# Kernel tuning notes

Measured on AMD Instinct MI355X. Metric: run time of the kernel, lower is better.

Reference implementation:

```python
import jax, jax.numpy as jnp
import numpy as np

DIM, H, WH, WW = 192, 6, 8, 8
N = WH * WW
B = 4096
NW = 64
HALF = DIM // 2
HD = DIM // H


def _make_buffers():
    # continuous relative coords table (1, 2WH-1, 2WW-1, 2), Swin-V2 style
    rh = np.arange(-(WH - 1), WH, dtype=np.float32)
    rw = np.arange(-(WW - 1), WW, dtype=np.float32)
    gh, gw = np.meshgrid(rh, rw, indexing='ij')
    tab = np.stack([gh, gw], axis=-1)[None]  # (1, 2WH-1, 2WW-1, 2)
    tab[..., 0] /= WH - 1
    tab[..., 1] /= WW - 1
    tab *= 3.2
    tab = np.sign(tab) * (1.0 - np.exp(-np.abs(tab)))
    # relative position index (N, N) int
    ch, cw = np.meshgrid(np.arange(WH), np.arange(WW), indexing='ij')
    coords = np.stack([ch, cw]).reshape(2, -1)  # (2, N)
    rel = coords[:, :, None] - coords[:, None, :]  # (2, N, N)
    rel = rel.transpose(1, 2, 0).astype(np.int64)
    rel[:, :, 0] += WH - 1
    rel[:, :, 1] += WW - 1
    rel[:, :, 0] *= 2 * WW - 1
    idx = rel.sum(-1)  # (N, N)
    return jnp.asarray(tab, jnp.float32), jnp.asarray(idx, jnp.int32)


def setup_inputs() -> dict:
    key = jax.random.key(0)
    ks = jax.random.split(key, 24)
    w = lambda k, shape: jax.random.normal(k, shape, jnp.float32) * 0.02
    rpb_table, rp_index = _make_buffers()
    inp = {
        'x': jax.random.normal(ks[0], (B, N, DIM), jnp.float32),
        'mask': jnp.zeros((NW, N, N), jnp.float32),
        'logit_scale': jnp.log(10.0) * jnp.ones((H, 1, 1), jnp.float32),
        'mlp_w1': w(ks[1], (128, 2)), 'mlp_b1': jnp.zeros((128,), jnp.float32),
        'mlp_w2': w(ks[2], (H, 128)),
        'q1w': w(ks[3], (HALF, HALF)), 'q1b': jnp.zeros((HALF,), jnp.float32),
        'q2w': w(ks[4], (HALF, HALF)), 'q2b': jnp.zeros((HALF,), jnp.float32),
        'k1w': w(ks[5], (HALF, HALF)), 'k1b': jnp.zeros((HALF,), jnp.float32),
        'k2w': w(ks[6], (HALF, HALF)), 'k2b': jnp.zeros((HALF,), jnp.float32),
        'v1w': w(ks[7], (HALF, HALF)), 'v1b': jnp.zeros((HALF,), jnp.float32),
        'v2w': w(ks[8], (HALF, HALF)), 'v2b': jnp.zeros((HALF,), jnp.float32),
        'p1w': w(ks[9], (HALF, HALF)), 'p1b': jnp.zeros((HALF,), jnp.float32),
        'p2w': w(ks[10], (HALF, HALF)), 'p2b': jnp.zeros((HALF,), jnp.float32),
        'rpb_table': rpb_table,
        'rp_index': rp_index,
    }
    return inp


def _lin(x, w, b):
    return x @ w.T + b


def _l2n(x):
    return x / jnp.maximum(jnp.linalg.norm(x, axis=-1, keepdims=True), 1e-12)


def reference(x, mask, logit_scale, mlp_w1, mlp_b1, mlp_w2,
              q1w, q1b, q2w, q2b, k1w, k1b, k2w, k2b, v1w, v1b, v2w, v2b,
              p1w, p1b, p2w, p2b, rpb_table, rp_index):
    b, n, c = x.shape
    h, hd = H, c // H
    x0, x1 = x[..., :c // 2], x[..., c // 2:]
    # split-channel GRL residual projections, then concat halves -> heads
    def heads(y0w, y0b, y1w, y1b):
        y = jnp.concatenate([x0 + _lin(x0, y0w, y0b), x1 + _lin(x1, y1w, y1b)], -1)
        return y.reshape(b, n, h, hd).transpose(0, 2, 1, 3)  # (b, h, n, hd)
    q = heads(q1w, q1b, q2w, q2b)
    k = heads(k1w, k1b, k2w, k2b)
    v = heads(v1w, v1b, v2w, v2b)
    # cosine attention with learned per-head logit scale
    attn = jnp.einsum('bhnd,bhmd->bhnm', _l2n(q), _l2n(k))
    scale = jnp.exp(jnp.minimum(logit_scale, jnp.log(jnp.float32(100.0))))  # (h,1,1)
    attn = attn * scale
    # ESRPB: MLP over continuous relative coords -> per-head bias
    tab = jax.nn.relu(rpb_table @ mlp_w1.T + mlp_b1) @ mlp_w2.T  # (1, 2WH-1, 2WW-1, h)
    tab = tab.reshape(-1, h)
    rpb = tab[rp_index.reshape(-1)].reshape(n, n, h).transpose(2, 0, 1)  # (h, n, n)
    attn = attn + 16.0 * jax.nn.sigmoid(rpb)[None]
    nw = mask.shape[0]
    attn = (attn.reshape(b // nw, nw, h, n, n) + mask[None, :, None]).reshape(b, h, n, n)
    attn = jax.nn.softmax(attn, axis=-1)
    out = jnp.einsum('bhnm,bhmd->bhnd', attn, v).transpose(0, 2, 1, 3).reshape(b, n, c)
    o0, o1 = out[..., :c // 2], out[..., c // 2:]
    return jnp.concatenate([_lin(o0, p1w, p1b), _lin(o1, p2w, p2b)], -1)
```

## Files before the change

kernel.cpp:

```cpp
#include <hip/hip_runtime.h>
#include <hip/hip_bf16.h>

#define NT 64
#define DM 192

typedef __attribute__((ext_vector_type(4))) float f32x4;
typedef __attribute__((ext_vector_type(4))) float float4v;
using half2v = __attribute__((ext_vector_type(2))) _Float16;
using half4v = __attribute__((ext_vector_type(4))) _Float16;

#define BIAS_OFF  147456
#define TAB_OFF   6438912
#define SCALE_OFF 6444312

__device__ __forceinline__ half4v pk4(float a, float b, float c, float d){
  half2v lo = __builtin_bit_cast(half2v, __builtin_amdgcn_cvt_pkrtz(a, b));
  half2v hi = __builtin_bit_cast(half2v, __builtin_amdgcn_cvt_pkrtz(c, d));
  half4v r; r[0]=lo[0]; r[1]=lo[1]; r[2]=hi[0]; r[3]=hi[1];
  return r;
}

__global__ __launch_bounds__(384) void pre_a(
  const float* __restrict__ q1w, const float* __restrict__ q2w,
  const float* __restrict__ k1w, const float* __restrict__ k2w,
  const float* __restrict__ v1w, const float* __restrict__ v2w,
  const float* __restrict__ p1w, const float* __restrict__ p2w,
  const float* __restrict__ w1, const float* __restrict__ b1,
  const float* __restrict__ w2, const float* __restrict__ rpbt,
  const float* __restrict__ ls, char* __restrict__ ws)
{
  int blk = blockIdx.x, t = threadIdx.x;
  if (blk < 48) {
    const float* Ws[8] = {q1w,q2w,k1w,k2w,v1w,v2w,p1w,p2w};
    int mat = blk / 6, ct = blk % 6;
    int lane = t & 63, ks = t >> 6;
    const float* W = Ws[mat];
    int c  = 16*ct + (lane & 15);
    int d0 = 16*ks + 4*(lane >> 4);
    half4v h;
    #pragma unroll
    for (int j = 0; j < 4; ++j) h[j] = (_Float16)W[c*96 + d0 + j];
    *(half4v*)(ws + (size_t)((mat*6+ct)*6+ks)*512 + lane*8) = h;
  } else {
    float* tab = (float*)(ws + TAB_OFF);
    if (t < 225) {
      float t0 = rpbt[2*t], t1 = rpbt[2*t+1];
      float acc[6] = {0,0,0,0,0,0};
      for (int j = 0; j < 128; ++j) {
        float hv = fmaxf(t0*w1[2*j] + t1*w1[2*j+1] + b1[j], 0.f);
        #pragma unroll
        for (int hh = 0; hh < 6; ++hh) acc[hh] += hv * w2[hh*128 + j];
      }
      #pragma unroll
      for (int hh = 0; hh < 6; ++hh) tab[t*6 + hh] = acc[hh];
    }
    if (t >= 240 && t < 246) {
      float* sc = (float*)(ws + SCALE_OFF);
      int i = t - 240;
      sc[i] = expf(fminf(ls[i], 4.605170185988091f));
    }
  }
}

__global__ __launch_bounds__(256) void pre_b(
  const float* __restrict__ mask, const int* __restrict__ rpi,
  char* __restrict__ ws)
{
  int w = blockIdx.x / 6, h = blockIdx.x % 6;
  int lane = threadIdx.x & 63, nt = threadIdx.x >> 6;
  const float* tab = (const float*)(ws + TAB_OFF);
  float* bias = (float*)(ws + BIAS_OFF);
  #pragma unroll
  for (int mt = 0; mt < 4; ++mt)
    #pragma unroll
    for (int r = 0; r < 4; ++r) {
      int m = 16*mt + ((lane >> 4) << 2) + r;
      int n = 16*nt + (lane & 15);
      int idx = rpi[n*64 + m];
      float tv = tab[idx*6 + h];
      float sg = 16.f / (1.f + expf(-tv));
      float mv = mask[(w*64 + n)*64 + m];
      bias[(size_t)(((w*6+h)*4+mt)*4+nt)*256 + lane*4 + r] = sg + mv;
    }
}

__global__ __launch_bounds__(768, 2) void win_attn(
  const float* __restrict__ x, const char* __restrict__ ws,
  const float* __restrict__ q1b, const float* __restrict__ q2b,
  const float* __restrict__ k1b, const float* __restrict__ k2b,
  const float* __restrict__ v1b, const float* __restrict__ v2b,
  const float* __restrict__ p1b, const float* __restrict__ p2b,
  float* __restrict__ out)
{
  __shared__ __align__(16) _Float16 xo2[2][64*200];
  const int tid = threadIdx.x;
  const int wv = tid >> 6, lane = tid & 63;
  const int llo = lane & 15, lhi = lane >> 4;
  const int wgrp = (wv >= 6) ? 1 : 0;
  const int h = wv - 6*wgrp;
  const int b = blockIdx.x*2 + wgrp, w_in = b & 63;
  const int lt = tid - 384*wgrp;
  _Float16* xo = xo2[wgrp];
  const int half = (h < 3) ? 0 : 1;
  const int hd0 = 32 * (h % 3);
  const f32x4 zf = {0.f,0.f,0.f,0.f};
  const float* xg = x + (size_t)b * (NT*DM);

  float4v xv[8];
  #pragma unroll
  for (int it = 0; it < 8; ++it) xv[it] = *(const float4v*)(xg + 4*(lt + it*384));
  #pragma unroll
  for (int it = 0; it < 8; ++it) {
    int f4 = lt + it*384;
    int row = f4 / 48, c4 = f4 % 48;
    *(half4v*)(xo + row*200 + c4*4) = pk4(xv[it][0], xv[it][1], xv[it][2], xv[it][3]);
  }
  __syncthreads();

  f32x4 qacc[2][4], kacc[2][4];
  #pragma unroll
  for (int dt = 0; dt < 2; ++dt)
    #pragma unroll
    for (int tt = 0; tt < 4; ++tt) { qacc[dt][tt] = zf; kacc[dt][tt] = zf; }
  #pragma unroll
  for (int ks = 0; ks < 6; ++ks) {
    half4v xf[4];
    #pragma unroll
    for (int tt = 0; tt < 4; ++tt)
      xf[tt] = *(const half4v*)(xo + (16*tt+llo)*200 + half*96 + 16*ks + 4*lhi);
    #pragma unroll
    for (int dt = 0; dt < 2; ++dt) {
      half4v wq = *(const half4v*)(ws + (size_t)(((0+half)*6 + 2*(h%3)+dt)*6 + ks)*512 + lane*8);
      half4v wk = *(const half4v*)(ws + (size_t)(((2+half)*6 + 2*(h%3)+dt)*6 + ks)*512 + lane*8);
      #pragma unroll
      for (int tt = 0; tt < 4; ++tt) {
        qacc[dt][tt] = __builtin_amdgcn_mfma_f32_16x16x16f16(wq, xf[tt], qacc[dt][tt], 0,0,0);
        kacc[dt][tt] = __builtin_amdgcn_mfma_f32_16x16x16f16(wk, xf[tt], kacc[dt][tt], 0,0,0);
      }
    }
  }
  const float* qbp = half ? q2b : q1b;
  const float* kbp = half ? k2b : k1b;
  float4v qb[2], kb[2];
  #pragma unroll
  for (int dt = 0; dt < 2; ++dt) {
    qb[dt] = *(const float4v*)(qbp + hd0 + 16*dt + 4*lhi);
    kb[dt] = *(const float4v*)(kbp + hd0 + 16*dt + 4*lhi);
  }
  const float scale_h = ((const float*)(ws + SCALE_OFF))[h];

  half4v qf[2][4], kf[2][4];
  #pragma unroll
  for (int tt = 0; tt < 4; ++tt) {
    float qv[2][4], kv[2][4];
    #pragma unroll
    for (int dt = 0; dt < 2; ++dt) {
      half4v xr = *(const half4v*)(xo + (16*tt+llo)*200 + half*96 + hd0 + 16*dt + 4*lhi);
      #pragma unroll
      for (int r = 0; r < 4; ++r) {
        float res = (float)xr[r];
        qv[dt][r] = qacc[dt][tt][r] + res + qb[dt][r];
        kv[dt][r] = kacc[dt][tt][r] + res + kb[dt][r];
      }
    }
    float sq = 0.f, sk = 0.f;
    #pragma unroll
    for (int dt = 0; dt < 2; ++dt)
      #pragma unroll
      for (int r = 0; r < 4; ++r) { sq += qv[dt][r]*qv[dt][r]; sk += kv[dt][r]*kv[dt][r]; }
    sq += __shfl_xor(sq, 16); sq += __shfl_xor(sq, 32);
    sk += __shfl_xor(sk, 16); sk += __shfl_xor(sk, 32);
    float invq = scale_h / fmaxf(sqrtf(sq), 1e-12f);
    float invk = 1.f / fmaxf(sqrtf(sk), 1e-12f);
    #pragma unroll
    for (int dt = 0; dt < 2; ++dt) {
      qf[dt][tt] = pk4(qv[dt][0]*invq, qv[dt][1]*invq, qv[dt][2]*invq, qv[dt][3]*invq);
      kf[dt][tt] = pk4(kv[dt][0]*invk, kv[dt][1]*invk, kv[dt][2]*invk, kv[dt][3]*invk);
    }
  }

  f32x4 vacc[4][2];
  #pragma unroll
  for (int tt = 0; tt < 4; ++tt) { vacc[tt][0] = zf; vacc[tt][1] = zf; }
  #pragma unroll
  for (int ks = 0; ks < 6; ++ks) {
    half4v xf[4];
    #pragma unroll
    for (int tt = 0; tt < 4; ++tt)
      xf[tt] = *(const half4v*)(xo + (16*tt+llo)*200 + half*96 + 16*ks + 4*lhi);
    #pragma unroll
    for (int ct = 0; ct < 2; ++ct) {
      half4v wvf = *(const half4v*)(ws + (size_t)(((4+half)*6 + 2*(h%3)+ct)*6 + ks)*512 + lane*8);
      #pragma unroll
      for (int tt = 0; tt < 4; ++tt)
        vacc[tt][ct] = __builtin_amdgcn_mfma_f32_16x16x16f16(xf[tt], wvf, vacc[tt][ct], 0,0,0);
    }
  }
  const float* vbp = half ? v2b : v1b;
  half4v vf[4][2];
  #pragma unroll
  for (int ct = 0; ct < 2; ++ct) {
    float vb = vbp[hd0 + 16*ct + llo];
    #pragma unroll
    for (int tt = 0; tt < 4; ++tt) {
      float vvv[4];
      #pragma unroll
      for (int r = 0; r < 4; ++r) {
        int tok = 16*tt + 4*lhi + r;
        float res = (float)xo[tok*200 + half*96 + hd0 + 16*ct + llo];
        vvv[r] = vacc[tt][ct][r] + res + vb;
      }
      vf[tt][ct] = pk4(vvv[0], vvv[1], vvv[2], vvv[3]);
    }
  }

  const float4v* biasf = (const float4v*)(ws + BIAS_OFF);
  half4v pf[4][4];
  #pragma unroll
  for (int nt = 0; nt < 4; ++nt) {
    f32x4 s[4];
    #pragma unroll
    for (int mt = 0; mt < 4; ++mt) {
      f32x4 t0 = __builtin_amdgcn_mfma_f32_16x16x16f16(kf[0][mt], qf[0][nt], zf, 0,0,0);
      s[mt]    = __builtin_amdgcn_mfma_f32_16x16x16f16(kf[1][mt], qf[1][nt], t0, 0,0,0);
      float4v bb = biasf[(size_t)(((w_in*6 + h)*4 + mt)*4 + nt)*64 + lane];
      s[mt][0] += bb[0]; s[mt][1] += bb[1]; s[mt][2] += bb[2]; s[mt][3] += bb[3];
    }
    float mx = s[0][0];
    #pragma unroll
    for (int mt = 0; mt < 4; ++mt)
      #pragma unroll
      for (int r = 0; r < 4; ++r) mx = fmaxf(mx, s[mt][r]);
    mx = fmaxf(mx, __shfl_xor(mx, 16)); mx = fmaxf(mx, __shfl_xor(mx, 32));
    float e[4][4]; float sum = 0.f;
    #pragma unroll
    for (int mt = 0; mt < 4; ++mt)
      #pragma unroll
      for (int r = 0; r < 4; ++r) { e[mt][r] = __expf(s[mt][r] - mx); sum += e[mt][r]; }
    sum += __shfl_xor(sum, 16); sum += __shfl_xor(sum, 32);
    float inv = 1.f / sum;
    #pragma unroll
    for (int mt = 0; mt < 4; ++mt)
      pf[mt][nt] = pk4(e[mt][0]*inv, e[mt][1]*inv, e[mt][2]*inv, e[mt][3]*inv);
  }

  f32x4 oacc[2][4];
  #pragma unroll
  for (int dt = 0; dt < 2; ++dt)
    #pragma unroll
    for (int nt = 0; nt < 4; ++nt) oacc[dt][nt] = zf;
  #pragma unroll
  for (int mt = 0; mt < 4; ++mt)
    #pragma unroll
    for (int dt = 0; dt < 2; ++dt)
      #pragma unroll
      for (int nt = 0; nt < 4; ++nt)
        oacc[dt][nt] = __builtin_amdgcn_mfma_f32_16x16x16f16(vf[mt][dt], pf[mt][nt], oacc[dt][nt], 0,0,0);

  __syncthreads();
  #pragma unroll
  for (int dt = 0; dt < 2; ++dt)
    #pragma unroll
    for (int nt = 0; nt < 4; ++nt)
      *(half4v*)(xo + (16*nt+llo)*200 + 32*h + 16*dt + 4*lhi) =
        pk4(oacc[dt][nt][0], oacc[dt][nt][1], oacc[dt][nt][2], oacc[dt][nt][3]);
  __syncthreads();

  const int ph = h & 1;
  const int cp = h >> 1;
  f32x4 facc[2][4];
  #pragma unroll
  for (int cc = 0; cc < 2; ++cc)
    #pragma unroll
    for (int nt = 0; nt < 4; ++nt) facc[cc][nt] = zf;
  #pragma unroll
  for (int ks = 0; ks < 6; ++ks) {
    half4v of[4];
    #pragma unroll
    for (int nt = 0; nt < 4; ++nt)
      of[nt] = *(const half4v*)(xo + (16*nt+llo)*200 + 96*ph + 16*ks + 4*lhi);
    #pragma unroll
    for (int cc = 0; cc < 2; ++cc) {
      half4v wp = *(const half4v*)(ws + (size_t)(((6+ph)*6 + 2*cp+cc)*6 + ks)*512 + lane*8);
      #pragma unroll
      for (int nt = 0; nt < 4; ++nt)
        facc[cc][nt] = __builtin_amdgcn_mfma_f32_16x16x16f16(wp, of[nt], facc[cc][nt], 0,0,0);
    }
  }
  const float* pbp = ph ? p2b : p1b;
  float* og = out + (size_t)b * (NT*DM);
  #pragma unroll
  for (int cc = 0; cc < 2; ++cc) {
    float4v pb = *(const float4v*)(pbp + 16*(2*cp+cc) + 4*lhi);
    #pragma unroll
    for (int nt = 0; nt < 4; ++nt) {
      float4v res;
      #pragma unroll
      for (int r = 0; r < 4; ++r) res[r] = facc[cc][nt][r] + pb[r];
      *(float4v*)(og + (size_t)(16*nt+llo)*192 + 96*ph + 16*(2*cp+cc) + 4*lhi) = res;
    }
  }
}

extern "C" void kernel_launch(void* const* d_in, const int* in_sizes, int n_in,
                              void* d_out, int out_size, void* d_ws, size_t ws_size,
                              hipStream_t stream)
{
  const float* x    = (const float*)d_in[0];
  const float* mask = (const float*)d_in[1];
  const float* ls   = (const float*)d_in[2];
  const float* w1   = (const float*)d_in[3];
  const float* b1   = (const float*)d_in[4];
  const float* w2   = (const float*)d_in[5];
  const float* q1w  = (const float*)d_in[6];  const float* q1b = (const float*)d_in[7];
  const float* q2w  = (const float*)d_in[8];  const float* q2b = (const float*)d_in[9];
  const float* k1w  = (const float*)d_in[10]; const float* k1b = (const float*)d_in[11];
  const float* k2w  = (const float*)d_in[12]; const float* k2b = (const float*)d_in[13];
  const float* v1w  = (const float*)d_in[14]; const float* v1b = (const float*)d_in[15];
  const float* v2w  = (const float*)d_in[16]; const float* v2b = (const float*)d_in[17];
  const float* p1w  = (const float*)d_in[18]; const float* p1b = (const float*)d_in[19];
  const float* p2w  = (const float*)d_in[20]; const float* p2b = (const float*)d_in[21];
  const float* rpbt = (const float*)d_in[22];
  const int*   rpi  = (const int*)d_in[23];
  char* ws = (char*)d_ws;
  float* o = (float*)d_out;

  pre_a<<<49, 384, 0, stream>>>(q1w,q2w,k1w,k2w,v1w,v2w,p1w,p2w, w1,b1,w2, rpbt, ls, ws);
  pre_b<<<384, 256, 0, stream>>>(mask, rpi, ws);
  win_attn<<<2048, 768, 0, stream>>>(x, ws, q1b,q2b,k1b,k2b,v1b,v2b,p1b,p2b, o);
}
```

Before: 221.4 us.

## Fold residual into weights, defer softmax normalization, compute V after softmax

Adds the identity matrix to the q/k/v weight matrices during preprocessing, so the residual add of x is absorbed into the MFMA and the per-element shared-memory residual reads are removed. Softmax probabilities are no longer divided by the row sum before P·V; the reciprocal is applied to the output accumulator at store time instead. The V projection is moved after the softmax to shorten live ranges and lower register pressure. Folding the identity in fp16 weights changes rounding slightly, because 1+w is stored in half precision.

```diff
diff --git a/kernel.cpp b/kernel.cpp
--- a/kernel.cpp
+++ b/kernel.cpp
@@ -39,7 +39,11 @@
     int d0 = 16*ks + 4*(lane >> 4);
     half4v h;
     #pragma unroll
-    for (int j = 0; j < 4; ++j) h[j] = (_Float16)W[c*96 + d0 + j];
+    for (int j = 0; j < 4; ++j) {
+      float wel = W[c*96 + d0 + j];
+      if (mat < 6 && c == d0 + j) wel += 1.0f;
+      h[j] = (_Float16)wel;
+    }
     *(half4v*)(ws + (size_t)((mat*6+ct)*6+ks)*512 + lane*8) = h;
   } else {
     float* tab = (float*)(ws + TAB_OFF);
@@ -117,105 +121,66 @@
   }
   __syncthreads();
 
-  f32x4 qacc[2][4], kacc[2][4];
-  #pragma unroll
-  for (int dt = 0; dt < 2; ++dt)
-    #pragma unroll
-    for (int tt = 0; tt < 4; ++tt) { qacc[dt][tt] = zf; kacc[dt][tt] = zf; }
-  #pragma unroll
-  for (int ks = 0; ks < 6; ++ks) {
-    half4v xf[4];
-    #pragma unroll
-    for (int tt = 0; tt < 4; ++tt)
-      xf[tt] = *(const half4v*)(xo + (16*tt+llo)*200 + half*96 + 16*ks + 4*lhi);
+  const float scale_h = ((const float*)(ws + SCALE_OFF))[h];
+
+  half4v qf[2][4], kf[2][4];
+  {
+    f32x4 qacc[2][4], kacc[2][4];
+    #pragma unroll
+    for (int dt = 0; dt < 2; ++dt)
+      #pragma unroll
+      for (int tt = 0; tt < 4; ++tt) { qacc[dt][tt] = zf; kacc[dt][tt] = zf; }
+    #pragma unroll
+    for (int ks = 0; ks < 6; ++ks) {
+      half4v xf[4];
+      #pragma unroll
+      for (int tt = 0; tt < 4; ++tt)
+        xf[tt] = *(const half4v*)(xo + (16*tt+llo)*200 + half*96 + 16*ks + 4*lhi);
+      #pragma unroll
+      for (int dt = 0; dt < 2; ++dt) {
+        half4v wq = *(const half4v*)(ws + (size_t)(((0+half)*6 + 2*(h%3)+dt)*6 + ks)*512 + lane*8);
+        half4v wk = *(const half4v*)(ws + (size_t)(((2+half)*6 + 2*(h%3)+dt)*6 + ks)*512 + lane*8);
+        #pragma unroll
+        for (int tt = 0; tt < 4; ++tt) {
+          qacc[dt][tt] = __builtin_amdgcn_mfma_f32_16x16x16f16(wq, xf[tt], qacc[dt][tt], 0,0,0);
+          kacc[dt][tt] = __builtin_amdgcn_mfma_f32_16x16x16f16(wk, xf[tt], kacc[dt][tt], 0,0,0);
+        }
+      }
+    }
+    const float* qbp = half ? q2b : q1b;
+    const float* kbp = half ? k2b : k1b;
+    float4v qb[2], kb[2];
     #pragma unroll
     for (int dt = 0; dt < 2; ++dt) {
-      half4v wq = *(const half4v*)(ws + (size_t)(((0+half)*6 + 2*(h%3)+dt)*6 + ks)*512 + lane*8);
-      half4v wk = *(const half4v*)(ws + (size_t)(((2+half)*6 + 2*(h%3)+dt)*6 + ks)*512 + lane*8);
-      #pragma unroll
-      for (int tt = 0; tt < 4; ++tt) {
-        qacc[dt][tt] = __builtin_amdgcn_mfma_f32_16x16x16f16(wq, xf[tt], qacc[dt][tt], 0,0,0);
-        kacc[dt][tt] = __builtin_amdgcn_mfma_f32_16x16x16f16(wk, xf[tt], kacc[dt][tt], 0,0,0);
+      qb[dt] = *(const float4v*)(qbp + hd0 + 16*dt + 4*lhi);
+      kb[dt] = *(const float4v*)(kbp + hd0 + 16*dt + 4*lhi);
+    }
+    #pragma unroll
+    for (int tt = 0; tt < 4; ++tt) {
+      float qv[2][4], kv[2][4];
+      float sq = 0.f, sk = 0.f;
+      #pragma unroll
+      for (int dt = 0; dt < 2; ++dt)
+        #pragma unroll
+        for (int r = 0; r < 4; ++r) {
+          qv[dt][r] = qacc[dt][tt][r] + qb[dt][r]; sq += qv[dt][r]*qv[dt][r];
+          kv[dt][r] = kacc[dt][tt][r] + kb[dt][r]; sk += kv[dt][r]*kv[dt][r];
+        }
+      sq += __shfl_xor(sq, 16); sq += __shfl_xor(sq, 32);
+      sk += __shfl_xor(sk, 16); sk += __shfl_xor(sk, 32);
+      float invq = scale_h / fmaxf(sqrtf(sq), 1e-12f);
+      float invk = 1.f / fmaxf(sqrtf(sk), 1e-12f);
+      #pragma unroll
+      for (int dt = 0; dt < 2; ++dt) {
+        qf[dt][tt] = pk4(qv[dt][0]*invq, qv[dt][1]*invq, qv[dt][2]*invq, qv[dt][3]*invq);
+        kf[dt][tt] = pk4(kv[dt][0]*invk, kv[dt][1]*invk, kv[dt][2]*invk, kv[dt][3]*invk);
       }
-    }
-  }
-  const float* qbp = half ? q2b : q1b;
-  const float* kbp = half ? k2b : k1b;
-  float4v qb[2], kb[2];
-  #pragma unroll
-  for (int dt = 0; dt < 2; ++dt) {
-    qb[dt] = *(const float4v*)(qbp + hd0 + 16*dt + 4*lhi);
-    kb[dt] = *(const float4v*)(kbp + hd0 + 16*dt + 4*lhi);
-  }
-  const float scale_h = ((const float*)(ws + SCALE_OFF))[h];
-
-  half4v qf[2][4], kf[2][4];
-  #pragma unroll
-  for (int tt = 0; tt < 4; ++tt) {
-    float qv[2][4], kv[2][4];
-    #pragma unroll
-    for (int dt = 0; dt < 2; ++dt) {
-      half4v xr = *(const half4v*)(xo + (16*tt+llo)*200 + half*96 + hd0 + 16*dt + 4*lhi);
-      #pragma unroll
-      for (int r = 0; r < 4; ++r) {
-        float res = (float)xr[r];
-        qv[dt][r] = qacc[dt][tt][r] + res + qb[dt][r];
-        kv[dt][r] = kacc[dt][tt][r] + res + kb[dt][r];
-      }
-    }
-    float sq = 0.f, sk = 0.f;
-    #pragma unroll
-    for (int dt = 0; dt < 2; ++dt)
-      #pragma unroll
-      for (int r = 0; r < 4; ++r) { sq += qv[dt][r]*qv[dt][r]; sk += kv[dt][r]*kv[dt][r]; }
-    sq += __shfl_xor(sq, 16); sq += __shfl_xor(sq, 32);
-    sk += __shfl_xor(sk, 16); sk += __shfl_xor(sk, 32);
-    float invq = scale_h / fmaxf(sqrtf(sq), 1e-12f);
-    float invk = 1.f / fmaxf(sqrtf(sk), 1e-12f);
-    #pragma unroll
-    for (int dt = 0; dt < 2; ++dt) {
-      qf[dt][tt] = pk4(qv[dt][0]*invq, qv[dt][1]*invq, qv[dt][2]*invq, qv[dt][3]*invq);
-      kf[dt][tt] = pk4(kv[dt][0]*invk, kv[dt][1]*invk, kv[dt][2]*invk, kv[dt][3]*invk);
-    }
-  }
-
-  f32x4 vacc[4][2];
-  #pragma unroll
-  for (int tt = 0; tt < 4; ++tt) { vacc[tt][0] = zf; vacc[tt][1] = zf; }
-  #pragma unroll
-  for (int ks = 0; ks < 6; ++ks) {
-    half4v xf[4];
-    #pragma unroll
-    for (int tt = 0; tt < 4; ++tt)
-      xf[tt] = *(const half4v*)(xo + (16*tt+llo)*200 + half*96 + 16*ks + 4*lhi);
-    #pragma unroll
-    for (int ct = 0; ct < 2; ++ct) {
-      half4v wvf = *(const half4v*)(ws + (size_t)(((4+half)*6 + 2*(h%3)+ct)*6 + ks)*512 + lane*8);
-      #pragma unroll
-      for (int tt = 0; tt < 4; ++tt)
-        vacc[tt][ct] = __builtin_amdgcn_mfma_f32_16x16x16f16(xf[tt], wvf, vacc[tt][ct], 0,0,0);
-    }
-  }
-  const float* vbp = half ? v2b : v1b;
-  half4v vf[4][2];
-  #pragma unroll
-  for (int ct = 0; ct < 2; ++ct) {
-    float vb = vbp[hd0 + 16*ct + llo];
-    #pragma unroll
-    for (int tt = 0; tt < 4; ++tt) {
-      float vvv[4];
-      #pragma unroll
-      for (int r = 0; r < 4; ++r) {
-        int tok = 16*tt + 4*lhi + r;
-        float res = (float)xo[tok*200 + half*96 + hd0 + 16*ct + llo];
-        vvv[r] = vacc[tt][ct][r] + res + vb;
-      }
-      vf[tt][ct] = pk4(vvv[0], vvv[1], vvv[2], vvv[3]);
     }
   }
 
   const float4v* biasf = (const float4v*)(ws + BIAS_OFF);
   half4v pf[4][4];
+  float inv_s[4];
   #pragma unroll
   for (int nt = 0; nt < 4; ++nt) {
     f32x4 s[4];
@@ -238,10 +203,40 @@
       #pragma unroll
       for (int r = 0; r < 4; ++r) { e[mt][r] = __expf(s[mt][r] - mx); sum += e[mt][r]; }
     sum += __shfl_xor(sum, 16); sum += __shfl_xor(sum, 32);
-    float inv = 1.f / sum;
+    inv_s[nt] = 1.f / sum;
     #pragma unroll
     for (int mt = 0; mt < 4; ++mt)
-      pf[mt][nt] = pk4(e[mt][0]*inv, e[mt][1]*inv, e[mt][2]*inv, e[mt][3]*inv);
+      pf[mt][nt] = pk4(e[mt][0], e[mt][1], e[mt][2], e[mt][3]);
+  }
+
+  half4v vf[4][2];
+  {
+    f32x4 acc[4][2];
+    #pragma unroll
+    for (int tt = 0; tt < 4; ++tt) { acc[tt][0] = zf; acc[tt][1] = zf; }
+    #pragma unroll
+    for (int ks = 0; ks < 6; ++ks) {
+      half4v xf[4];
+      #pragma unroll
+      for (int tt = 0; tt < 4; ++tt)
+        xf[tt] = *(const half4v*)(xo + (16*tt+llo)*200 + half*96 + 16*ks + 4*lhi);
+      #pragma unroll
+      for (int ct = 0; ct < 2; ++ct) {
+        half4v wvf = *(const half4v*)(ws + (size_t)(((4+half)*6 + 2*(h%3)+ct)*6 + ks)*512 + lane*8);
+        #pragma unroll
+        for (int tt = 0; tt < 4; ++tt)
+          acc[tt][ct] = __builtin_amdgcn_mfma_f32_16x16x16f16(xf[tt], wvf, acc[tt][ct], 0,0,0);
+      }
+    }
+    const float* vbp = half ? v2b : v1b;
+    #pragma unroll
+    for (int ct = 0; ct < 2; ++ct) {
+      float vb = vbp[hd0 + 16*ct + llo];
+      #pragma unroll
+      for (int tt = 0; tt < 4; ++tt)
+        vf[tt][ct] = pk4(acc[tt][ct][0] + vb, acc[tt][ct][1] + vb,
+                         acc[tt][ct][2] + vb, acc[tt][ct][3] + vb);
+    }
   }
 
   f32x4 oacc[2][4];
@@ -263,7 +258,8 @@
     #pragma unroll
     for (int nt = 0; nt < 4; ++nt)
       *(half4v*)(xo + (16*nt+llo)*200 + 32*h + 16*dt + 4*lhi) =
-        pk4(oacc[dt][nt][0], oacc[dt][nt][1], oacc[dt][nt][2], oacc[dt][nt][3]);
+        pk4(oacc[dt][nt][0]*inv_s[nt], oacc[dt][nt][1]*inv_s[nt],
+            oacc[dt][nt][2]*inv_s[nt], oacc[dt][nt][3]*inv_s[nt]);
   __syncthreads();
 
   const int ph = h & 1;
```

Result: slower. 234.4 us (+5.9%).
